# Performance work log

Hardware: AMD Instinct MI355X
Metric: run time of the kernel (lower is better)

The kernel has to match this reference:

```python
import jax, jax.numpy as jnp
import numpy as np

B, T, IN, D = 32, 1024, 1536, 768


def setup_inputs() -> dict:
    key = jax.random.key(0)
    ks = jax.random.split(key, 14)
    s_in = 1.0 / np.sqrt(IN)
    s_d = 1.0 / np.sqrt(D)
    return {
        "x": jax.random.normal(ks[0], (B, T, IN), jnp.float32),
        # fc1/fc2 torch Linear weights stored [out, in]
        "fc1_w": jax.random.normal(ks[1], (IN, IN), jnp.float32) * s_in,
        "fc1_b": jax.random.normal(ks[2], (IN,), jnp.float32) * 0.01,
        "fc2_w": jax.random.normal(ks[3], (D, IN), jnp.float32) * s_in,
        "fc2_b": jax.random.normal(ks[4], (D,), jnp.float32) * 0.01,
        # Unary: Conv1d(D,D,k=1) then Conv1d(D,1,k=1); k=1 conv == per-token linear
        "un_emb_w": jax.random.normal(ks[5], (D, D), jnp.float32) * s_d,
        "un_emb_b": jax.random.normal(ks[6], (D,), jnp.float32) * 0.01,
        "un_red_w": jax.random.normal(ks[7], (1, D), jnp.float32) * s_d,
        "un_red_b": jax.random.normal(ks[8], (1,), jnp.float32) * 0.01,
        # Self Pairwise: x_embedding / y_embedding Conv1d(D,D,k=1)
        "pw_x_w": jax.random.normal(ks[9], (D, D), jnp.float32) * s_d,
        "pw_x_b": jax.random.normal(ks[10], (D,), jnp.float32) * 0.01,
        "pw_y_w": jax.random.normal(ks[11], (D, D), jnp.float32) * s_d,
        "pw_y_b": jax.random.normal(ks[12], (D,), jnp.float32) * 0.01,
        # reduce_potentials: Conv1d(2,1,k=1,bias=False) -> 2 scalars
        "red_w": jax.random.normal(ks[13], (2,), jnp.float32),
    }


def reference(x, fc1_w, fc1_b, fc2_w, fc2_b,
              un_emb_w, un_emb_b, un_red_w, un_red_b,
              pw_x_w, pw_x_b, pw_y_w, pw_y_b, red_w):
    # FGAEmbedder MLP: fc2(relu(fc1(x)))
    h = jax.nn.relu(jnp.einsum('bti,oi->bto', x, fc1_w) + fc1_b)
    u = jnp.einsum('bti,oi->bto', h, fc2_w) + fc2_b            # [B,T,D]

    # Unary potential (dropout is identity at inference)
    e = jax.nn.relu(jnp.einsum('btd,od->bto', u, un_emb_w) + un_emb_b)
    un_pot = (jnp.einsum('btd,od->bto', e, un_red_w) + un_red_b)[..., 0]  # [B,T]

    # Self pairwise: cosine-similarity matrix, marginalized by mean (spatial_dim=None)
    xe = jnp.einsum('btd,od->bto', u, pw_x_w) + pw_x_b
    ye = jnp.einsum('btd,od->bto', u, pw_y_w) + pw_y_b
    xn = xe / jnp.maximum(jnp.linalg.norm(xe, axis=-1, keepdims=True), 1e-12)
    yn = ye / jnp.maximum(jnp.linalg.norm(ye, axis=-1, keepdims=True), 1e-12)
    S = jnp.einsum('btd,bsd->bts', xn, yn)                     # [B,T,T]
    pw_pot = jnp.mean(S, axis=2)                               # [B,T]

    # reduce potentials (Conv1d 2->1 no bias; order: unary then self), softmax attention
    scores = red_w[0] * un_pot + red_w[1] * pw_pot             # [B,T]
    w = jax.nn.softmax(scores, axis=1)
    return jnp.einsum('btd,bt->bd', u, w)                      # [B,D]
```

## Files before the change

### kernel.cpp

```cpp
#include <hip/hip_runtime.h>
#include <stdint.h>

#define MROWS 32768
#define TSEQ  1024
#define BBATCH 32
#define INDIM 1536
#define DDIM  768
#define NCAT  2304

typedef short short8 __attribute__((ext_vector_type(8)));
typedef short short4v __attribute__((ext_vector_type(4)));
typedef float f32x4  __attribute__((ext_vector_type(4)));

__device__ __forceinline__ float b2f(ushort u) {
    union { uint32_t u; float f; } x; x.u = ((uint32_t)u) << 16; return x.f;
}
__device__ __forceinline__ ushort f2b(float f) {
    union { float f; uint32_t u; } x; x.f = f;
    uint32_t r = x.u + 0x7fffu + ((x.u >> 16) & 1u);
    return (ushort)(r >> 16);
}

__device__ __forceinline__ void cvt4(const float* __restrict__ in, ushort* __restrict__ out, int i) {
    float4 v = ((const float4*)in)[i];
    ushort4 o;
    o.x = f2b(v.x); o.y = f2b(v.y); o.z = f2b(v.z); o.w = f2b(v.w);
    ((ushort4*)out)[i] = o;
}

#define C0 12582912
#define C1 13172736
#define C2 13467648
#define C3 13615104
#define C4 13762560
#define C5 13910016
#define C6 13910592
#define C7 13916736
#define C8 13922880
#define C9 13947456
__global__ void cvt_all(const float* __restrict__ x,
                        const float* __restrict__ fc1_w, const float* __restrict__ fc2_w,
                        const float* __restrict__ w3a, const float* __restrict__ w3b,
                        const float* __restrict__ w3c,
                        const float* __restrict__ ba, const float* __restrict__ bb,
                        const float* __restrict__ bc,
                        ushort* __restrict__ X16, ushort* __restrict__ W1,
                        ushort* __restrict__ W2, ushort* __restrict__ W3,
                        float* __restrict__ B3, float* __restrict__ ybar_z,
                        float* __restrict__ out_z, float* __restrict__ stats_z)
{
    int i = blockIdx.x * 256 + threadIdx.x;
    float4 z = {0.f, 0.f, 0.f, 0.f};
    if (i < C0)       cvt4(x, X16, i);
    else if (i < C1)  cvt4(fc1_w, W1, i - C0);
    else if (i < C2)  cvt4(fc2_w, W2, i - C1);
    else if (i < C3)  cvt4(w3a, W3,           i - C2);
    else if (i < C4)  cvt4(w3b, W3 + 589824,  i - C3);
    else if (i < C5)  cvt4(w3c, W3 + 1179648, i - C4);
    else if (i < C6) {
        int j = i - C5;
        const float* src = (j < 192) ? ba : (j < 384) ? bb : bc;
        int off = (j < 192) ? j : (j < 384) ? (j - 192) : (j - 384);
        ((float4*)B3)[j] = ((const float4*)src)[off];
    }
    else if (i < C7)  ((float4*)ybar_z)[i - C6] = z;
    else if (i < C8)  ((float4*)out_z)[i - C7] = z;
    else if (i < C9)  ((float4*)stats_z)[i - C8] = z;
}

__global__ __launch_bounds__(512, 2)
void gemm_bt(const ushort* __restrict__ A, const ushort* __restrict__ Bm,
             const float* __restrict__ bias, ushort* __restrict__ C,
             int M, int N, int K, int relu_ncols,
             const float* __restrict__ urw, float* __restrict__ SE,
             float* __restrict__ SX, float* __restrict__ SY)
{
    __shared__ __align__(16) ushort lds[65536];

    const int tid  = threadIdx.x;
    const int lane = tid & 63, wave = tid >> 6;
    const int wm = wave >> 2, wn = wave & 3;
    const int quad = lane >> 4, r16 = lane & 15;

    const int ntiles = N >> 8;
    const int xcd = blockIdx.x & 7;
    const int j   = blockIdx.x >> 3;
    const int g   = j / ntiles;
    const int n_t = j - g * ntiles;
    const int m_t = xcd + (g << 3);
    const int m0 = m_t * 256, n0 = n_t * 256;

    const int srow = lane >> 2;
    const int sgr  = (lane & 3) ^ ((lane >> 3) & 3);
    const int goff = (r16 << 5) + ((quad ^ ((r16 >> 1) & 3)) << 3);

    const ushort* gA = A  + (size_t)(m0 + wave * 32 + srow) * K + sgr * 8;
    const ushort* gB = Bm + (size_t)(n0 + wave * 32 + srow) * K + sgr * 8;
    const int ldsA = wave * 1024;
    const int ldsB = 8192 + wave * 1024;

    const int kT = K >> 5;

#define STAGE(p, off) __builtin_amdgcn_global_load_lds( \
        (const __attribute__((address_space(1))) void*)(p), \
        (__attribute__((address_space(3))) void*)&lds[off], 16, 0, 0)

    for (int t = 0; t < 3; ++t) {
        const int bufb = t << 14;
        const ushort* a = gA + (size_t)t * 32;
        const ushort* b = gB + (size_t)t * 32;
        STAGE(a,                  bufb + ldsA);
        STAGE(a + (size_t)16 * K, bufb + ldsA + 512);
        STAGE(b,                  bufb + ldsB);
        STAGE(b + (size_t)16 * K, bufb + ldsB + 512);
    }

    f32x4 acc[8][4] = {};

    asm volatile("s_waitcnt vmcnt(8)" ::: "memory");
    asm volatile("s_barrier" ::: "memory");

    for (int t = 0; t < kT; ++t) {
        const int bufb = (t & 3) << 14;
        const ushort* sa = &lds[bufb + (wm << 12) + goff];
        const ushort* sb = &lds[bufb + 8192 + (wn << 11) + goff];
        short8 af[4], bf[4];

#pragma unroll
        for (int i = 0; i < 4; ++i)  af[i] = *(const short8*)(sa + i * 512);
#pragma unroll
        for (int jj = 0; jj < 4; ++jj) bf[jj] = *(const short8*)(sb + jj * 512);
        if (t + 3 < kT) {
            const int nb = ((t + 3) & 3) << 14;
            STAGE(gA + (size_t)(t + 3) * 32, nb + ldsA);
            STAGE(gB + (size_t)(t + 3) * 32, nb + ldsB);
        }
        asm volatile("s_barrier" ::: "memory");
        asm volatile("s_waitcnt lgkmcnt(0)" ::: "memory");
        __builtin_amdgcn_s_setprio(1);
#pragma unroll
        for (int i = 0; i < 4; ++i)
#pragma unroll
            for (int jj = 0; jj < 4; ++jj)
                acc[i][jj] = __builtin_amdgcn_mfma_f32_16x16x32_bf16(af[i], bf[jj], acc[i][jj], 0, 0, 0);
        __builtin_amdgcn_s_setprio(0);
        asm volatile("s_barrier" ::: "memory");

#pragma unroll
        for (int i = 0; i < 4; ++i)  af[i] = *(const short8*)(sa + (4 + i) * 512);
        if (t + 3 < kT) {
            const int nb = ((t + 3) & 3) << 14;
            STAGE(gA + (size_t)(t + 3) * 32 + (size_t)16 * K, nb + ldsA + 512);
            STAGE(gB + (size_t)(t + 3) * 32 + (size_t)16 * K, nb + ldsB + 512);
        }
        if (t < kT - 3)       asm volatile("s_waitcnt vmcnt(8)" ::: "memory");
        else if (t == kT - 3) asm volatile("s_waitcnt vmcnt(4)" ::: "memory");
        else if (t == kT - 2) asm volatile("s_waitcnt vmcnt(0)" ::: "memory");
        asm volatile("s_barrier" ::: "memory");
        asm volatile("s_waitcnt lgkmcnt(0)" ::: "memory");
        __builtin_amdgcn_s_setprio(1);
#pragma unroll
        for (int i = 0; i < 4; ++i)
#pragma unroll
            for (int jj = 0; jj < 4; ++jj)
                acc[4 + i][jj] = __builtin_amdgcn_mfma_f32_16x16x32_bf16(af[i], bf[jj], acc[4 + i][jj], 0, 0, 0);
        __builtin_amdgcn_s_setprio(0);
        asm volatile("s_barrier" ::: "memory");
    }
#undef STAGE

    const bool stats = (urw != nullptr);
    const int sec = n0 / DDIM;
    float st[8][4] = {};
#pragma unroll
    for (int jj = 0; jj < 4; ++jj) {
        int gn = n0 + wn * 64 + jj * 16 + r16;
        float bv = bias[gn];
        bool dorelu = gn < relu_ncols;
        float uw = (stats && sec == 0) ? urw[gn] : 0.f;
#pragma unroll
        for (int i = 0; i < 8; ++i) {
            int gmb = m0 + wm * 128 + i * 16 + quad * 4;
#pragma unroll
            for (int rr = 0; rr < 4; ++rr) {
                float v = acc[i][jj][rr] + bv;
                if (dorelu) v = fmaxf(v, 0.f);
                C[(size_t)(gmb + rr) * N + gn] = f2b(v);
                if (stats) st[i][rr] += (sec == 0) ? v * uw : v * v;
            }
        }
    }
    if (stats) {
#pragma unroll
        for (int i = 0; i < 8; ++i)
#pragma unroll
            for (int rr = 0; rr < 4; ++rr) {
                float v = st[i][rr];
                v += __shfl_xor(v, 1, 64);
                v += __shfl_xor(v, 2, 64);
                v += __shfl_xor(v, 4, 64);
                v += __shfl_xor(v, 8, 64);
                st[i][rr] = v;
            }
        if (r16 == 0) {
            float* dst = (sec == 0) ? SE : (sec == 1) ? SX : SY;
#pragma unroll
            for (int i = 0; i < 8; ++i)
#pragma unroll
                for (int rr = 0; rr < 4; ++rr)
                    atomicAdd(&dst[m0 + wm * 128 + i * 16 + quad * 4 + rr], st[i][rr]);
        }
    }
}

__global__ void ybar_k(const ushort* __restrict__ G3, const float* __restrict__ sy,
                       float* __restrict__ ybar)
{
    int b = blockIdx.x, s0 = blockIdx.y * 32;
    int tid = threadIdx.x;
    __shared__ float sr[32];
    if (tid < 32) {
        float v = sy[b * TSEQ + s0 + tid];
        sr[tid] = (1.0f / TSEQ) / fmaxf(sqrtf(v), 1e-12f);
    }
    __syncthreads();
    float a0 = 0.f, a1 = 0.f, a2 = 0.f;
#pragma unroll 8
    for (int s = 0; s < 32; ++s) {
        const ushort* row = G3 + (size_t)(b * TSEQ + s0 + s) * NCAT + 2 * DDIM;
        float w = sr[s];
        a0 += b2f(row[tid])       * w;
        a1 += b2f(row[tid + 256]) * w;
        a2 += b2f(row[tid + 512]) * w;
    }
    atomicAdd(&ybar[b * DDIM + tid],       a0);
    atomicAdd(&ybar[b * DDIM + tid + 256], a1);
    atomicAdd(&ybar[b * DDIM + tid + 512], a2);
}

__global__ void pw_scores_k(const ushort* __restrict__ G3, const float* __restrict__ ybar,
                            const float* __restrict__ SE, const float* __restrict__ SX,
                            const float* __restrict__ urb, const float* __restrict__ red_w,
                            float* __restrict__ scores)
{
    int wv = threadIdx.x >> 6, lane = threadIdx.x & 63;
    int m = blockIdx.x * 4 + wv;
    int b = m >> 10;
    const ushort* xe = G3 + (size_t)m * NCAT + DDIM;
    const float4* yb = (const float4*)(ybar + b * DDIM);
    float s = 0.f;
#pragma unroll
    for (int c0 = 0; c0 < 3; ++c0) {
        int c = lane + c0 * 64;
        short4v v = *(const short4v*)(xe + c * 4);
        float4 yv = yb[c];
        s += b2f((ushort)v[0]) * yv.x + b2f((ushort)v[1]) * yv.y
           + b2f((ushort)v[2]) * yv.z + b2f((ushort)v[3]) * yv.w;
    }
#pragma unroll
    for (int off = 32; off; off >>= 1) s += __shfl_xor(s, off, 64);
    if (lane == 0) {
        float rnx = 1.f / fmaxf(sqrtf(SX[m]), 1e-12f);
        scores[m] = red_w[0] * (SE[m] + urb[0]) + red_w[1] * (rnx * s);
    }
}

__global__ void out_sm_k(const ushort* __restrict__ U16, const float* __restrict__ scores,
                         float* __restrict__ out)
{
    int b = blockIdx.x, t0 = blockIdx.y * 32;
    int tid = threadIdx.x;
    int lane = tid & 63, wv = tid >> 6;
    __shared__ float red[8];
    __shared__ float sw[32];

    float v[4];
    float lm = -1e30f;
#pragma unroll
    for (int i = 0; i < 4; ++i) {
        v[i] = scores[b * TSEQ + i * 256 + tid];
        lm = fmaxf(lm, v[i]);
    }
#pragma unroll
    for (int off = 32; off; off >>= 1) lm = fmaxf(lm, __shfl_xor(lm, off, 64));
    if (lane == 0) red[wv] = lm;
    __syncthreads();
    float smax = fmaxf(fmaxf(red[0], red[1]), fmaxf(red[2], red[3]));
    float ls = 0.f;
#pragma unroll
    for (int i = 0; i < 4; ++i) ls += expf(v[i] - smax);
#pragma unroll
    for (int off = 32; off; off >>= 1) ls += __shfl_xor(ls, off, 64);
    if (lane == 0) red[4 + wv] = ls;
    __syncthreads();
    float inv = 1.f / (red[4] + red[5] + red[6] + red[7]);

    if (tid < 32) sw[tid] = expf(scores[b * TSEQ + t0 + tid] - smax) * inv;
    __syncthreads();

    float a0 = 0.f, a1 = 0.f, a2 = 0.f;
#pragma unroll 8
    for (int t = 0; t < 32; ++t) {
        const ushort* row = U16 + (size_t)(b * TSEQ + t0 + t) * DDIM;
        float w = sw[t];
        a0 += b2f(row[tid])       * w;
        a1 += b2f(row[tid + 256]) * w;
        a2 += b2f(row[tid + 512]) * w;
    }
    atomicAdd(&out[b * DDIM + tid],       a0);
    atomicAdd(&out[b * DDIM + tid + 256], a1);
    atomicAdd(&out[b * DDIM + tid + 512], a2);
}

static const size_t O_X16   = 0;
static const size_t O_H16   = 100663296;
static const size_t O_G3    = 0;
static const size_t O_U16   = 201326592;
static const size_t O_W1    = 251658240;
static const size_t O_W2    = 256376832;
static const size_t O_W3    = 258736128;
static const size_t O_B3    = 262275072;
static const size_t O_SE    = 262284288;
static const size_t O_SX    = 262415360;
static const size_t O_SY    = 262546432;
static const size_t O_SCORE = 262677504;
static const size_t O_YBAR  = 262939648;

extern "C" void kernel_launch(void* const* d_in, const int* in_sizes, int n_in,
                              void* d_out, int out_size, void* d_ws, size_t ws_size,
                              hipStream_t stream)
{
    const float* x        = (const float*)d_in[0];
    const float* fc1_w    = (const float*)d_in[1];
    const float* fc1_b    = (const float*)d_in[2];
    const float* fc2_w    = (const float*)d_in[3];
    const float* fc2_b    = (const float*)d_in[4];
    const float* un_emb_w = (const float*)d_in[5];
    const float* un_emb_b = (const float*)d_in[6];
    const float* un_red_w = (const float*)d_in[7];
    const float* un_red_b = (const float*)d_in[8];
    const float* pw_x_w   = (const float*)d_in[9];
    const float* pw_x_b   = (const float*)d_in[10];
    const float* pw_y_w   = (const float*)d_in[11];
    const float* pw_y_b   = (const float*)d_in[12];
    const float* red_w    = (const float*)d_in[13];

    char* ws = (char*)d_ws;
    ushort* X16 = (ushort*)(ws + O_X16);
    ushort* H16 = (ushort*)(ws + O_H16);
    ushort* G3  = (ushort*)(ws + O_G3);
    ushort* U16 = (ushort*)(ws + O_U16);
    ushort* W1  = (ushort*)(ws + O_W1);
    ushort* W2  = (ushort*)(ws + O_W2);
    ushort* W3  = (ushort*)(ws + O_W3);
    float*  B3  = (float*)(ws + O_B3);
    float*  SE  = (float*)(ws + O_SE);
    float*  SX  = (float*)(ws + O_SX);
    float*  SY  = (float*)(ws + O_SY);
    float*  SCORES = (float*)(ws + O_SCORE);
    float*  YBAR = (float*)(ws + O_YBAR);

    cvt_all<<<54483, 256, 0, stream>>>(x, fc1_w, fc2_w, un_emb_w, pw_x_w, pw_y_w,
                                       un_emb_b, pw_x_b, pw_y_b,
                                       X16, W1, W2, W3, B3, YBAR, (float*)d_out, SE);

    gemm_bt<<<(MROWS / 256) * (INDIM / 256), 512, 0, stream>>>(
        X16, W1, fc1_b, H16, MROWS, INDIM, INDIM, INDIM,
        nullptr, nullptr, nullptr, nullptr);
    gemm_bt<<<(MROWS / 256) * (DDIM / 256), 512, 0, stream>>>(
        H16, W2, fc2_b, U16, MROWS, DDIM, INDIM, 0,
        nullptr, nullptr, nullptr, nullptr);
    gemm_bt<<<(MROWS / 256) * (NCAT / 256), 512, 0, stream>>>(
        U16, W3, B3, G3, MROWS, NCAT, DDIM, DDIM,
        un_red_w, SE, SX, SY);

    ybar_k<<<dim3(BBATCH, 32), 256, 0, stream>>>(G3, SY, YBAR);
    pw_scores_k<<<MROWS / 4, 256, 0, stream>>>(G3, YBAR, SE, SX, un_red_b, red_w, SCORES);
    out_sm_k<<<dim3(BBATCH, 32), 256, 0, stream>>>(U16, SCORES, (float*)d_out);
}
```

Before: 771.9 us.

## Restructure GEMM main loop to K=64 steps with split A/B staging buffers

The bf16 GEMM mainloop moves from K=32 steps with a 4-deep unified buffer to K=64 steps. A now has a triple buffer and B a double buffer, with loads interleaved across four MFMA sub-phases per iteration. This halves the iteration and barrier count per K and spreads global-to-LDS staging more evenly between MFMA bursts. LDS use grows to 160KB per block, and the epilogue loop is reordered so stores run row-major across columns. The larger LDS footprint may cut occupancy against the launch bounds of 2 blocks, and the hand-tuned waitcnt logic is fragile.

```diff
diff --git a/kernel.cpp b/kernel.cpp
--- a/kernel.cpp
+++ b/kernel.cpp
@@ -75,7 +75,7 @@
              const float* __restrict__ urw, float* __restrict__ SE,
              float* __restrict__ SX, float* __restrict__ SY)
 {
-    __shared__ __align__(16) ushort lds[65536];
+    __shared__ __align__(16) ushort lds[81920];
 
     const int tid  = threadIdx.x;
     const int lane = tid & 63, wave = tid >> 6;
@@ -91,102 +91,147 @@
     const int m0 = m_t * 256, n0 = n_t * 256;
 
     const int srow = lane >> 2;
-    const int sgr  = (lane & 3) ^ ((lane >> 3) & 3);
+    const int g8   = (((lane & 3) ^ ((srow >> 1) & 3)) << 3);
     const int goff = (r16 << 5) + ((quad ^ ((r16 >> 1) & 3)) << 3);
 
-    const ushort* gA = A  + (size_t)(m0 + wave * 32 + srow) * K + sgr * 8;
-    const ushort* gB = Bm + (size_t)(n0 + wave * 32 + srow) * K + sgr * 8;
-    const int ldsA = wave * 1024;
-    const int ldsB = 8192 + wave * 1024;
-
-    const int kT = K >> 5;
-
-#define STAGE(p, off) __builtin_amdgcn_global_load_lds( \
+    const ushort* pA = A + (size_t)(m0 + (wave & 3) * 16 + srow + (wave >> 2) * 128) * K + g8;
+    const int segA = (((wave >> 2) * 8 + (wave & 3)) << 9) + lane * 8;
+    const ushort* pB = Bm + (size_t)(n0 + (wave >> 1) * 64 + (wave & 1) * 16 + srow) * K + g8;
+    const int segB = (((wave >> 1) * 4 + (wave & 1)) << 9) + lane * 8;
+
+    const int kT = K >> 6;
+
+#define STG(p, off) __builtin_amdgcn_global_load_lds( \
         (const __attribute__((address_space(1))) void*)(p), \
         (__attribute__((address_space(3))) void*)&lds[off], 16, 0, 0)
-
-    for (int t = 0; t < 3; ++t) {
-        const int bufb = t << 14;
-        const ushort* a = gA + (size_t)t * 32;
-        const ushort* b = gB + (size_t)t * 32;
-        STAGE(a,                  bufb + ldsA);
-        STAGE(a + (size_t)16 * K, bufb + ldsA + 512);
-        STAGE(b,                  bufb + ldsB);
-        STAGE(b + (size_t)16 * K, bufb + ldsB + 512);
-    }
+#define STAGE_A(tt, MH) do { \
+        const ushort* s_ = pA + (size_t)(MH) * 64 * K + (size_t)(tt) * 64; \
+        const int d_ = ((tt) % 3) * 16384 + (MH) * 2048 + segA; \
+        STG(s_,      d_); \
+        STG(s_ + 32, d_ + 8192); } while (0)
+#define STAGE_B(tt, NH) do { \
+        const ushort* s_ = pB + (size_t)(NH) * 32 * K + (size_t)(tt) * 64; \
+        const int d_ = 49152 + ((tt) & 1) * 16384 + (NH) * 1024 + segB; \
+        STG(s_,      d_); \
+        STG(s_ + 32, d_ + 8192); } while (0)
+
+    STAGE_A(0, 0); STAGE_A(0, 1);
+    STAGE_B(0, 0); STAGE_B(0, 1);
+    STAGE_A(1, 0); STAGE_A(1, 1);
+    asm volatile("s_waitcnt vmcnt(4)" ::: "memory");
+    asm volatile("s_barrier" ::: "memory");
 
     f32x4 acc[8][4] = {};
-
-    asm volatile("s_waitcnt vmcnt(8)" ::: "memory");
-    asm volatile("s_barrier" ::: "memory");
+    short8 af0[2][4], af1[2][4], bf[2][2];
 
     for (int t = 0; t < kT; ++t) {
-        const int bufb = (t & 3) << 14;
-        const ushort* sa = &lds[bufb + (wm << 12) + goff];
-        const ushort* sb = &lds[bufb + 8192 + (wn << 11) + goff];
-        short8 af[4], bf[4];
-
-#pragma unroll
-        for (int i = 0; i < 4; ++i)  af[i] = *(const short8*)(sa + i * 512);
-#pragma unroll
-        for (int jj = 0; jj < 4; ++jj) bf[jj] = *(const short8*)(sb + jj * 512);
-        if (t + 3 < kT) {
-            const int nb = ((t + 3) & 3) << 14;
-            STAGE(gA + (size_t)(t + 3) * 32, nb + ldsA);
-            STAGE(gB + (size_t)(t + 3) * 32, nb + ldsB);
+        const int aB = (t % 3) * 16384;
+        const int bB = 49152 + (t & 1) * 16384;
+        const bool stB = (t + 1 < kT), stA = (t + 2 < kT);
+
+#pragma unroll
+        for (int ks = 0; ks < 2; ++ks) {
+#pragma unroll
+            for (int i = 0; i < 4; ++i)
+                af0[ks][i] = *(const short8*)&lds[aB + ks * 8192 + (wm * 8 + i) * 512 + goff];
+#pragma unroll
+            for (int jj = 0; jj < 2; ++jj)
+                bf[ks][jj] = *(const short8*)&lds[bB + ks * 8192 + (wn * 4 + jj) * 512 + goff];
         }
+        if (stB) STAGE_B(t + 1, 0);
         asm volatile("s_barrier" ::: "memory");
         asm volatile("s_waitcnt lgkmcnt(0)" ::: "memory");
         __builtin_amdgcn_s_setprio(1);
 #pragma unroll
         for (int i = 0; i < 4; ++i)
 #pragma unroll
-            for (int jj = 0; jj < 4; ++jj)
-                acc[i][jj] = __builtin_amdgcn_mfma_f32_16x16x32_bf16(af[i], bf[jj], acc[i][jj], 0, 0, 0);
+            for (int jj = 0; jj < 2; ++jj) {
+                acc[i][jj] = __builtin_amdgcn_mfma_f32_16x16x32_bf16(af0[0][i], bf[0][jj], acc[i][jj], 0, 0, 0);
+                acc[i][jj] = __builtin_amdgcn_mfma_f32_16x16x32_bf16(af0[1][i], bf[1][jj], acc[i][jj], 0, 0, 0);
+            }
         __builtin_amdgcn_s_setprio(0);
         asm volatile("s_barrier" ::: "memory");
 
 #pragma unroll
-        for (int i = 0; i < 4; ++i)  af[i] = *(const short8*)(sa + (4 + i) * 512);
-        if (t + 3 < kT) {
-            const int nb = ((t + 3) & 3) << 14;
-            STAGE(gA + (size_t)(t + 3) * 32 + (size_t)16 * K, nb + ldsA + 512);
-            STAGE(gB + (size_t)(t + 3) * 32 + (size_t)16 * K, nb + ldsB + 512);
-        }
-        if (t < kT - 3)       asm volatile("s_waitcnt vmcnt(8)" ::: "memory");
-        else if (t == kT - 3) asm volatile("s_waitcnt vmcnt(4)" ::: "memory");
-        else if (t == kT - 2) asm volatile("s_waitcnt vmcnt(0)" ::: "memory");
+        for (int ks = 0; ks < 2; ++ks)
+#pragma unroll
+            for (int i = 0; i < 4; ++i)
+                af1[ks][i] = *(const short8*)&lds[aB + ks * 8192 + (wm * 8 + 4 + i) * 512 + goff];
+        if (stB) STAGE_B(t + 1, 1);
         asm volatile("s_barrier" ::: "memory");
         asm volatile("s_waitcnt lgkmcnt(0)" ::: "memory");
         __builtin_amdgcn_s_setprio(1);
 #pragma unroll
         for (int i = 0; i < 4; ++i)
 #pragma unroll
-            for (int jj = 0; jj < 4; ++jj)
-                acc[4 + i][jj] = __builtin_amdgcn_mfma_f32_16x16x32_bf16(af[i], bf[jj], acc[4 + i][jj], 0, 0, 0);
+            for (int jj = 0; jj < 2; ++jj) {
+                acc[4 + i][jj] = __builtin_amdgcn_mfma_f32_16x16x32_bf16(af1[0][i], bf[0][jj], acc[4 + i][jj], 0, 0, 0);
+                acc[4 + i][jj] = __builtin_amdgcn_mfma_f32_16x16x32_bf16(af1[1][i], bf[1][jj], acc[4 + i][jj], 0, 0, 0);
+            }
         __builtin_amdgcn_s_setprio(0);
         asm volatile("s_barrier" ::: "memory");
-    }
-#undef STAGE
+
+#pragma unroll
+        for (int ks = 0; ks < 2; ++ks)
+#pragma unroll
+            for (int jj = 0; jj < 2; ++jj)
+                bf[ks][jj] = *(const short8*)&lds[bB + ks * 8192 + (wn * 4 + 2 + jj) * 512 + goff];
+        if (stA) STAGE_A(t + 2, 0);
+        asm volatile("s_barrier" ::: "memory");
+        asm volatile("s_waitcnt lgkmcnt(0)" ::: "memory");
+        __builtin_amdgcn_s_setprio(1);
+#pragma unroll
+        for (int i = 0; i < 4; ++i)
+#pragma unroll
+            for (int jj = 0; jj < 2; ++jj) {
+                acc[4 + i][2 + jj] = __builtin_amdgcn_mfma_f32_16x16x32_bf16(af1[0][i], bf[0][jj], acc[4 + i][2 + jj], 0, 0, 0);
+                acc[4 + i][2 + jj] = __builtin_amdgcn_mfma_f32_16x16x32_bf16(af1[1][i], bf[1][jj], acc[4 + i][2 + jj], 0, 0, 0);
+            }
+        __builtin_amdgcn_s_setprio(0);
+        asm volatile("s_barrier" ::: "memory");
+
+        if (stA) STAGE_A(t + 2, 1);
+        if (t + 3 <= kT)      asm volatile("s_waitcnt vmcnt(4)" ::: "memory");
+        else if (t == kT - 2) asm volatile("s_waitcnt vmcnt(0)" ::: "memory");
+        asm volatile("s_barrier" ::: "memory");
+        __builtin_amdgcn_s_setprio(1);
+#pragma unroll
+        for (int i = 0; i < 4; ++i)
+#pragma unroll
+            for (int jj = 0; jj < 2; ++jj) {
+                acc[i][2 + jj] = __builtin_amdgcn_mfma_f32_16x16x32_bf16(af0[0][i], bf[0][jj], acc[i][2 + jj], 0, 0, 0);
+                acc[i][2 + jj] = __builtin_amdgcn_mfma_f32_16x16x32_bf16(af0[1][i], bf[1][jj], acc[i][2 + jj], 0, 0, 0);
+            }
+        __builtin_amdgcn_s_setprio(0);
+        asm volatile("s_barrier" ::: "memory");
+    }
+#undef STAGE_A
+#undef STAGE_B
+#undef STG
 
     const bool stats = (urw != nullptr);
     const int sec = n0 / DDIM;
-    float st[8][4] = {};
+    float bv[4], uwv[4];
+    bool dr[4];
 #pragma unroll
     for (int jj = 0; jj < 4; ++jj) {
         int gn = n0 + wn * 64 + jj * 16 + r16;
-        float bv = bias[gn];
-        bool dorelu = gn < relu_ncols;
-        float uw = (stats && sec == 0) ? urw[gn] : 0.f;
-#pragma unroll
-        for (int i = 0; i < 8; ++i) {
-            int gmb = m0 + wm * 128 + i * 16 + quad * 4;
-#pragma unroll
-            for (int rr = 0; rr < 4; ++rr) {
-                float v = acc[i][jj][rr] + bv;
-                if (dorelu) v = fmaxf(v, 0.f);
-                C[(size_t)(gmb + rr) * N + gn] = f2b(v);
-                if (stats) st[i][rr] += (sec == 0) ? v * uw : v * v;
+        bv[jj] = bias[gn];
+        dr[jj] = gn < relu_ncols;
+        uwv[jj] = (stats && sec == 0) ? urw[gn] : 0.f;
+    }
+    float st[8][4] = {};
+#pragma unroll
+    for (int i = 0; i < 8; ++i) {
+#pragma unroll
+        for (int rr = 0; rr < 4; ++rr) {
+            size_t base = (size_t)(m0 + wm * 128 + i * 16 + quad * 4 + rr) * N + n0 + wn * 64 + r16;
+#pragma unroll
+            for (int jj = 0; jj < 4; ++jj) {
+                float v = acc[i][jj][rr] + bv[jj];
+                if (dr[jj]) v = fmaxf(v, 0.f);
+                C[base + jj * 16] = f2b(v);
+                if (stats) st[i][rr] += (sec == 0) ? v * uwv[jj] : v * v;
             }
         }
     }
```

After: 733.5 us. -5.0%, faster.
